# Kernel optimization log

Hardware: AMD Instinct MI355X
Metric: run time of the kernel (lower is better)

The kernel has to match this reference:

```python
import jax, jax.numpy as jnp
import numpy as np

TOP_K = 32

def setup_inputs() -> dict:
    key = jax.random.key(0)
    x = jax.random.normal(key, (4096, 32768), dtype=jnp.float32)
    return {"x": x}

def reference(x) -> jnp.ndarray:
    bsz, d_sae = x.shape
    k = min(TOP_K, d_sae)
    # top-k indices per row (unsorted order does not matter for masking)
    _, idxs = jax.lax.top_k(x, k)  # [batch, k]
    rows = jnp.arange(bsz)[:, None]  # [batch, 1]
    mask = jnp.zeros_like(x).at[rows, idxs].set(1.0)
    return mask * x
```

## Files before the change

kernel.cpp:

```cpp
#include <hip/hip_runtime.h>

#define TOPK    32
#define ROW     32768
#define THREADS 512
#define WAVES   8
#define VPT     16
#define BINS    2048
#define CAP     1024

__device__ __forceinline__ unsigned int f2key(float f) {
    unsigned int u = __float_as_uint(f);
    return u ^ (0x80000000u | (unsigned int)((int)u >> 31));
}
__device__ __forceinline__ float key2f(unsigned int k) {
    unsigned int u = (k & 0x80000000u) ? (k & 0x7fffffffu) : ~k;
    return __uint_as_float(u);
}

__device__ __forceinline__ void bar_lds() {
    asm volatile("s_waitcnt lgkmcnt(0)" ::: "memory");
    __builtin_amdgcn_s_barrier();
}

struct Shared {
    unsigned int hist[BINS];
    unsigned int wsum[WAVES];
    unsigned int sel_g, sel_gabove;
    unsigned int sel_bin, sel_above;
    unsigned int cand_cnt;
    unsigned int cnt_s;
    float        cf[CAP];
    unsigned int cidx[CAP];
};

__device__ __forceinline__ void hist_select(Shared& sh, int t, int lane,
                                            int wave, unsigned int kk) {
    const int base = wave * 256 + lane * 4;
    unsigned int h0 = sh.hist[base + 0], h1 = sh.hist[base + 1];
    unsigned int h2 = sh.hist[base + 2], h3 = sh.hist[base + 3];
    unsigned int p = h0 + h1 + h2 + h3;
    unsigned int s = p;
#pragma unroll
    for (int off = 1; off < 64; off <<= 1) {
        unsigned int vv = __shfl_down(s, off);
        if (lane + off < 64) s += vv;
    }
    if (lane == 0) sh.wsum[wave] = s;
    bar_lds();

    if (t == 0) {
        unsigned int above = 0; int g = WAVES - 1;
        for (int w = WAVES - 1; w >= 0; --w) {
            if (above + sh.wsum[w] >= kk) { g = w; break; }
            above += sh.wsum[w];
        }
        sh.sel_g = (unsigned int)g; sh.sel_gabove = above;
    }
    bar_lds();

    if (wave == (int)sh.sel_g) {
        unsigned int a = sh.sel_gabove + (s - p);
        unsigned int hh[4] = {h0, h1, h2, h3};
#pragma unroll
        for (int j = 3; j >= 0; --j) {
            unsigned int h = hh[j];
            if (a < kk && a + h >= kk) {
                sh.sel_bin = (unsigned int)(base + j);
                sh.sel_above = a;
            }
            a += h;
        }
    }
    bar_lds();
}

__global__ __launch_bounds__(THREADS, 4) void topk_eager_kernel(
    const float* __restrict__ x, float* __restrict__ out) {

    __shared__ Shared sh;
    const int row  = blockIdx.x;
    const int t    = threadIdx.x;
    const int lane = t & 63;
    const int wave = t >> 6;

    const float4* __restrict__ xin =
        reinterpret_cast<const float4*>(x + (size_t)row * ROW);
    float4* __restrict__ xout =
        reinterpret_cast<float4*>(out + (size_t)row * ROW);
    float* __restrict__ orow = out + (size_t)row * ROW;

    float4 v[VPT];
    const float4 z4 = make_float4(0.f, 0.f, 0.f, 0.f);
#pragma unroll
    for (int i = 0; i < VPT; ++i) {
        v[i] = xin[i * THREADS + t];
        xout[i * THREADS + t] = z4;
    }
    __builtin_amdgcn_sched_barrier(0);

#pragma unroll
    for (int b = 0; b < BINS / THREADS; ++b) sh.hist[t + b * THREADS] = 0;
    if (t == 0) sh.cand_cnt = 0;

    float m = -__builtin_inff();
#pragma unroll
    for (int i = 0; i < VPT; ++i)
        m = fmaxf(m, fmaxf(fmaxf(v[i].x, v[i].y), fmaxf(v[i].z, v[i].w)));

    bar_lds();
    atomicAdd(&sh.hist[f2key(m) >> 21], 1u);
    bar_lds();

    hist_select(sh, t, lane, wave, TOPK);

    const float L = key2f(sh.sel_bin << 21);

#pragma unroll
    for (int i = 0; i < VPT; ++i) {
#pragma unroll
        for (int j = 0; j < 4; ++j) {
            float f = (&v[i].x)[j];
            if (f >= L) {
                unsigned int pos = atomicAdd(&sh.cand_cnt, 1u);
                if (pos < CAP) {
                    sh.cf[pos]   = f;
                    sh.cidx[pos] = (unsigned int)((i * THREADS + t) * 4 + j);
                }
            }
        }
    }
    bar_lds();
    const unsigned int C = sh.cand_cnt;

    if (C <= CAP) {
        float        wv[2];
        unsigned int wi[2];
        int nw = 0;
        for (unsigned int i = t; i < C; i += THREADS) {
            float ki = sh.cf[i]; unsigned int ii = sh.cidx[i];
            unsigned int r = 0;
            for (unsigned int j = 0; j < C; ++j) {
                float kj = sh.cf[j];
                unsigned int ij = sh.cidx[j];
                r += (kj > ki || (kj == ki && ij < ii)) ? 1u : 0u;
            }
            if (r < TOPK) { wv[nw] = ki; wi[nw] = ii; ++nw; }
        }
        __syncthreads();
        for (int q = 0; q < nw; ++q) orow[wi[q]] = wv[q];
        return;
    }

    unsigned int prefix = 0; int pbits = 0;
    unsigned int kk = TOPK, e = 0;
    for (int r = 0; r < 3; ++r) {
        const int shift = (r == 0) ? 21 : (r == 1 ? 10 : 0);
        const int bits  = (r == 2) ? 10 : 11;
        const unsigned int msk = (1u << bits) - 1u;
        bar_lds();
#pragma unroll
        for (int b = 0; b < BINS / THREADS; ++b) sh.hist[t + b * THREADS] = 0;
        bar_lds();
#pragma unroll
        for (int i = 0; i < VPT; ++i) {
#pragma unroll
            for (int j = 0; j < 4; ++j) {
                unsigned int key = f2key((&v[i].x)[j]);
                bool match = (pbits == 0) || ((key >> (32 - pbits)) == prefix);
                if (match) atomicAdd(&sh.hist[(key >> shift) & msk], 1u);
            }
        }
        bar_lds();
        hist_select(sh, t, lane, wave, kk);
        kk = kk - sh.sel_above;
        e  = sh.hist[sh.sel_bin];
        prefix = (prefix << bits) | sh.sel_bin;
        pbits += bits;
    }
    const unsigned int T = prefix;

    unsigned int Cc = ROW;
    if (e != kk) {
        unsigned int lo = 0, hi = ROW;
        while (hi - lo > 1u) {
            unsigned int mid = (lo + hi) >> 1;
            bar_lds();
            if (t == 0) sh.cnt_s = 0;
            bar_lds();
            unsigned int c = 0;
#pragma unroll
            for (int i = 0; i < VPT; ++i) {
#pragma unroll
                for (int j = 0; j < 4; ++j) {
                    unsigned int key = f2key((&v[i].x)[j]);
                    unsigned int idx = (unsigned int)((i * THREADS + t) * 4 + j);
                    if (key == T && idx < mid) ++c;
                }
            }
            if (c) atomicAdd(&sh.cnt_s, c);
            bar_lds();
            if (sh.cnt_s >= kk) hi = mid; else lo = mid;
        }
        Cc = hi;
    }

    __syncthreads();
#pragma unroll
    for (int i = 0; i < VPT; ++i) {
        float4 o;
#pragma unroll
        for (int j = 0; j < 4; ++j) {
            float f = (&v[i].x)[j];
            unsigned int key = f2key(f);
            unsigned int idx = (unsigned int)((i * THREADS + t) * 4 + j);
            (&o.x)[j] = (key > T || (key == T && idx < Cc)) ? f : 0.0f;
        }
        xout[i * THREADS + t] = o;
    }
}

extern "C" void kernel_launch(void* const* d_in, const int* in_sizes, int n_in,
                              void* d_out, int out_size, void* d_ws, size_t ws_size,
                              hipStream_t stream) {
    const float* x = (const float*)d_in[0];
    float* out = (float*)d_out;
    const int rows = in_sizes[0] / ROW;
    topk_eager_kernel<<<rows, THREADS, 0, stream>>>(x, out);
}
```

Before: 224.9 us.

## Split each row across two blocks with a workspace merge kernel

Each row is processed by two 256-thread blocks, one per half of the row. Each block zeroes its output half, finds that half's local top-32 as (key, index) pairs and writes them to workspace, and a second small kernel merges the 64 candidates per row by rank and scatters the winners. The goal is more blocks and parallelism per row, at the cost of an extra launch, workspace traffic and ordering between the zero-fill and the scatter. A single-kernel fallback is kept for when the workspace is too small, but its over-capacity path approximates the threshold and can be wrong.

```diff
diff --git a/kernel.cpp b/kernel.cpp
--- a/kernel.cpp
+++ b/kernel.cpp
@@ -2,18 +2,21 @@
 
 #define TOPK    32
 #define ROW     32768
-#define THREADS 512
-#define WAVES   8
+#define HALF    16384
+#define THREADS 256
+#define WAVES   4
 #define VPT     16
 #define BINS    2048
 #define CAP     1024
 
-__device__ __forceinline__ unsigned int f2key(float f) {
-    unsigned int u = __float_as_uint(f);
-    return u ^ (0x80000000u | (unsigned int)((int)u >> 31));
-}
-__device__ __forceinline__ float key2f(unsigned int k) {
-    unsigned int u = (k & 0x80000000u) ? (k & 0x7fffffffu) : ~k;
+typedef unsigned int u32;
+
+__device__ __forceinline__ u32 f2key(float f) {
+    u32 u = __float_as_uint(f);
+    return u ^ (0x80000000u | (u32)((int)u >> 31));
+}
+__device__ __forceinline__ float key2f(u32 k) {
+    u32 u = (k & 0x80000000u) ? (k & 0x7fffffffu) : ~k;
     return __uint_as_float(u);
 }
 
@@ -22,200 +25,319 @@
     __builtin_amdgcn_s_barrier();
 }
 
-struct Shared {
-    unsigned int hist[BINS];
-    unsigned int wsum[WAVES];
-    unsigned int sel_g, sel_gabove;
-    unsigned int sel_bin, sel_above;
-    unsigned int cand_cnt;
-    unsigned int cnt_s;
-    float        cf[CAP];
-    unsigned int cidx[CAP];
+struct SharedH {
+    u32 hist[BINS];
+    u32 wsum[WAVES];
+    u32 sel_g, sel_gabove;
+    u32 sel_bin, sel_above;
+    u32 cand_cnt;
+    u32 win_cnt;
+    u32 cnt_s;
+    u32 ckey[CAP];
+    u32 cidx[CAP];
 };
 
-__device__ __forceinline__ void hist_select(Shared& sh, int t, int lane,
-                                            int wave, unsigned int kk) {
-    const int base = wave * 256 + lane * 4;
-    unsigned int h0 = sh.hist[base + 0], h1 = sh.hist[base + 1];
-    unsigned int h2 = sh.hist[base + 2], h3 = sh.hist[base + 3];
-    unsigned int p = h0 + h1 + h2 + h3;
-    unsigned int s = p;
+__device__ __forceinline__ void hist_select(SharedH& sh, int t, int lane,
+                                            int wave, u32 kk) {
+    const int base = wave * 512 + lane * 8;
+    u32 h[8]; u32 p = 0;
+#pragma unroll
+    for (int j = 0; j < 8; ++j) { h[j] = sh.hist[base + j]; p += h[j]; }
+    u32 s = p;
 #pragma unroll
     for (int off = 1; off < 64; off <<= 1) {
-        unsigned int vv = __shfl_down(s, off);
+        u32 vv = __shfl_down(s, off);
         if (lane + off < 64) s += vv;
     }
     if (lane == 0) sh.wsum[wave] = s;
     bar_lds();
 
     if (t == 0) {
-        unsigned int above = 0; int g = WAVES - 1;
+        u32 above = 0; int g = WAVES - 1;
         for (int w = WAVES - 1; w >= 0; --w) {
             if (above + sh.wsum[w] >= kk) { g = w; break; }
             above += sh.wsum[w];
         }
-        sh.sel_g = (unsigned int)g; sh.sel_gabove = above;
+        sh.sel_g = (u32)g; sh.sel_gabove = above;
     }
     bar_lds();
 
     if (wave == (int)sh.sel_g) {
-        unsigned int a = sh.sel_gabove + (s - p);
-        unsigned int hh[4] = {h0, h1, h2, h3};
-#pragma unroll
-        for (int j = 3; j >= 0; --j) {
-            unsigned int h = hh[j];
-            if (a < kk && a + h >= kk) {
-                sh.sel_bin = (unsigned int)(base + j);
+        u32 a = sh.sel_gabove + (s - p);
+#pragma unroll
+        for (int j = 7; j >= 0; --j) {
+            u32 hh = h[j];
+            if (a < kk && a + hh >= kk) {
+                sh.sel_bin = (u32)(base + j);
                 sh.sel_above = a;
             }
-            a += h;
-        }
-    }
-    bar_lds();
-}
-
-__global__ __launch_bounds__(THREADS, 4) void topk_eager_kernel(
+            a += hh;
+        }
+    }
+    bar_lds();
+}
+
+__global__ __launch_bounds__(THREADS, 4) void topk_half_kernel(
+    const float* __restrict__ x, float* __restrict__ out,
+    uint2* __restrict__ ws) {
+
+    __shared__ SharedH sh;
+    const int hb      = blockIdx.x;
+    const int row     = hb >> 1;
+    const int halfsel = hb & 1;
+    const int t       = threadIdx.x;
+    const int lane    = t & 63;
+    const int wave    = t >> 6;
+    const size_t base_off = (size_t)row * ROW + (size_t)halfsel * HALF;
+
+    const float4* __restrict__ xin  = (const float4*)(x + base_off);
+    float4*       __restrict__ xout = (float4*)(out + base_off);
+
+    float4 v[VPT];
+    const float4 z4 = make_float4(0.f, 0.f, 0.f, 0.f);
+#pragma unroll
+    for (int i = 0; i < VPT; ++i) {
+        v[i] = xin[i * THREADS + t];
+        xout[i * THREADS + t] = z4;
+    }
+    __builtin_amdgcn_sched_barrier(0);
+
+#pragma unroll
+    for (int b = 0; b < BINS / THREADS; ++b) sh.hist[t + b * THREADS] = 0;
+    if (t == 0) { sh.cand_cnt = 0; sh.win_cnt = 0; }
+
+    float m = -__builtin_inff();
+#pragma unroll
+    for (int i = 0; i < VPT; ++i)
+        m = fmaxf(m, fmaxf(fmaxf(v[i].x, v[i].y), fmaxf(v[i].z, v[i].w)));
+
+    bar_lds();
+    atomicAdd(&sh.hist[f2key(m) >> 21], 1u);
+    bar_lds();
+
+    hist_select(sh, t, lane, wave, TOPK);
+
+    const u32 Lk = sh.sel_bin << 21;
+
+#pragma unroll
+    for (int i = 0; i < VPT; ++i) {
+#pragma unroll
+        for (int j = 0; j < 4; ++j) {
+            u32 key = f2key((&v[i].x)[j]);
+            if (key >= Lk) {
+                u32 pos = atomicAdd(&sh.cand_cnt, 1u);
+                if (pos < CAP) {
+                    sh.ckey[pos] = key;
+                    sh.cidx[pos] = (u32)((i * THREADS + t) * 4 + j);
+                }
+            }
+        }
+    }
+    bar_lds();
+    const u32 C = sh.cand_cnt;
+    uint2* __restrict__ wrow = ws + (size_t)hb * TOPK;
+
+    if (C <= CAP) {
+        for (u32 i = t; i < C; i += THREADS) {
+            u32 ki = sh.ckey[i], ii = sh.cidx[i];
+            u32 r = 0;
+            for (u32 j = 0; j < C; ++j) {
+                u32 kj = sh.ckey[j], ij = sh.cidx[j];
+                r += (kj > ki || (kj == ki && ij < ii)) ? 1u : 0u;
+            }
+            if (r < TOPK) {
+                u32 slot = atomicAdd(&sh.win_cnt, 1u);
+                wrow[slot] = make_uint2(ki, ii + (u32)halfsel * HALF);
+            }
+        }
+        return;
+    }
+
+    u32 prefix = 0; int pbits = 0;
+    u32 kk = TOPK, e = 0;
+    for (int r = 0; r < 3; ++r) {
+        const int shift = (r == 0) ? 21 : (r == 1 ? 10 : 0);
+        const int bits  = (r == 2) ? 10 : 11;
+        const u32 msk = (1u << bits) - 1u;
+        __syncthreads();
+#pragma unroll
+        for (int b = 0; b < BINS / THREADS; ++b) sh.hist[t + b * THREADS] = 0;
+        __syncthreads();
+#pragma unroll
+        for (int i = 0; i < VPT; ++i) {
+#pragma unroll
+            for (int j = 0; j < 4; ++j) {
+                u32 key = f2key((&v[i].x)[j]);
+                bool match = (pbits == 0) || ((key >> (32 - pbits)) == prefix);
+                if (match) atomicAdd(&sh.hist[(key >> shift) & msk], 1u);
+            }
+        }
+        __syncthreads();
+        if (t == 0) {
+            u32 above = 0;
+            const int nb = 1 << bits;
+            for (int b = nb - 1; b >= 0; --b) {
+                u32 h = sh.hist[b];
+                if (above + h >= kk) { sh.sel_bin = (u32)b;
+                                       sh.sel_above = above; break; }
+                above += h;
+            }
+        }
+        __syncthreads();
+        kk -= sh.sel_above;
+        e = sh.hist[sh.sel_bin];
+        prefix = (prefix << bits) | sh.sel_bin;
+        pbits += bits;
+        __syncthreads();
+    }
+    const u32 T = prefix;
+
+    u32 Cc = HALF;
+    if (e != kk) {
+        u32 lo = 0, hi = HALF;
+        while (hi - lo > 1u) {
+            u32 mid = (lo + hi) >> 1;
+            __syncthreads();
+            if (t == 0) sh.cnt_s = 0;
+            __syncthreads();
+            u32 c = 0;
+#pragma unroll
+            for (int i = 0; i < VPT; ++i) {
+#pragma unroll
+                for (int j = 0; j < 4; ++j) {
+                    u32 key = f2key((&v[i].x)[j]);
+                    u32 idx = (u32)((i * THREADS + t) * 4 + j);
+                    if (key == T && idx < mid) ++c;
+                }
+            }
+            if (c) atomicAdd(&sh.cnt_s, c);
+            __syncthreads();
+            if (sh.cnt_s >= kk) hi = mid; else lo = mid;
+        }
+        Cc = hi;
+    }
+
+#pragma unroll
+    for (int i = 0; i < VPT; ++i) {
+#pragma unroll
+        for (int j = 0; j < 4; ++j) {
+            u32 key = f2key((&v[i].x)[j]);
+            u32 idx = (u32)((i * THREADS + t) * 4 + j);
+            if (key > T || (key == T && idx < Cc)) {
+                u32 slot = atomicAdd(&sh.win_cnt, 1u);
+                wrow[slot] = make_uint2(key, idx + (u32)halfsel * HALF);
+            }
+        }
+    }
+}
+
+__global__ __launch_bounds__(64, 8) void topk_merge_kernel(
+    const uint2* __restrict__ ws, float* __restrict__ out) {
+
+    __shared__ u32 bk[64], bi[64];
+    const int row = blockIdx.x;
+    const int l   = threadIdx.x;
+
+    uint2 e = ws[(size_t)row * 64 + l];
+    bk[l] = e.x; bi[l] = e.y;
+    __syncthreads();
+
+    u32 r = 0;
+#pragma unroll
+    for (int j = 0; j < 64; ++j) {
+        u32 kj = bk[j], ij = bi[j];
+        r += (kj > e.x || (kj == e.x && ij < e.y)) ? 1u : 0u;
+    }
+    if (r < TOPK) out[(size_t)row * ROW + e.y] = key2f(e.x);
+}
+
+__global__ __launch_bounds__(512, 4) void topk_full_kernel(
     const float* __restrict__ x, float* __restrict__ out) {
 
-    __shared__ Shared sh;
+    __shared__ SharedH sh;
     const int row  = blockIdx.x;
     const int t    = threadIdx.x;
     const int lane = t & 63;
     const int wave = t >> 6;
 
-    const float4* __restrict__ xin =
+    const float4* __restrict__ xin  =
         reinterpret_cast<const float4*>(x + (size_t)row * ROW);
     float4* __restrict__ xout =
         reinterpret_cast<float4*>(out + (size_t)row * ROW);
-    float* __restrict__ orow = out + (size_t)row * ROW;
 
     float4 v[VPT];
-    const float4 z4 = make_float4(0.f, 0.f, 0.f, 0.f);
-#pragma unroll
-    for (int i = 0; i < VPT; ++i) {
-        v[i] = xin[i * THREADS + t];
-        xout[i * THREADS + t] = z4;
-    }
-    __builtin_amdgcn_sched_barrier(0);
-
-#pragma unroll
-    for (int b = 0; b < BINS / THREADS; ++b) sh.hist[t + b * THREADS] = 0;
+#pragma unroll
+    for (int i = 0; i < VPT; ++i) v[i] = xin[i * 512 + t];
+
+    for (int b = t; b < BINS; b += 512) sh.hist[b] = 0;
     if (t == 0) sh.cand_cnt = 0;
+    __syncthreads();
 
     float m = -__builtin_inff();
 #pragma unroll
     for (int i = 0; i < VPT; ++i)
         m = fmaxf(m, fmaxf(fmaxf(v[i].x, v[i].y), fmaxf(v[i].z, v[i].w)));
-
-    bar_lds();
     atomicAdd(&sh.hist[f2key(m) >> 21], 1u);
-    bar_lds();
-
-    hist_select(sh, t, lane, wave, TOPK);
-
-    const float L = key2f(sh.sel_bin << 21);
-
-#pragma unroll
-    for (int i = 0; i < VPT; ++i) {
+    __syncthreads();
+
+    if (t == 0) {
+        u32 above = 0;
+        for (int b = BINS - 1; b >= 0; --b) {
+            u32 h = sh.hist[b];
+            if (above + h >= TOPK) { sh.sel_bin = (u32)b; break; }
+            above += h;
+        }
+    }
+    __syncthreads();
+    const u32 Lk = sh.sel_bin << 21;
+
+#pragma unroll
+    for (int i = 0; i < VPT; ++i) {
+#pragma unroll
+        for (int j = 0; j < 4; ++j) {
+            u32 key = f2key((&v[i].x)[j]);
+            if (key >= Lk) {
+                u32 pos = atomicAdd(&sh.cand_cnt, 1u);
+                if (pos < CAP) {
+                    sh.ckey[pos] = key;
+                    sh.cidx[pos] = (u32)((i * 512 + t) * 4 + j);
+                }
+            }
+        }
+    }
+    __syncthreads();
+    const u32 C = sh.cand_cnt;
+    u32 Tk = 0, ic = 0;
+    if (C <= CAP) {
+        for (u32 i = t; i < C; i += 512) {
+            u32 ki = sh.ckey[i], ii = sh.cidx[i];
+            u32 r = 0;
+            for (u32 j = 0; j < C; ++j) {
+                u32 kj = sh.ckey[j], ij = sh.cidx[j];
+                r += (kj > ki || (kj == ki && ij < ii)) ? 1u : 0u;
+            }
+            if (r == TOPK - 1) { sh.sel_g = ki; sh.sel_gabove = ii; }
+        }
+        __syncthreads();
+        Tk = sh.sel_g; ic = sh.sel_gabove;
+    } else {
+        if (t == 0) {
+            sh.sel_g = Lk; sh.sel_gabove = ROW;
+        }
+        __syncthreads();
+        Tk = sh.sel_g; ic = sh.sel_gabove;
+    }
+#pragma unroll
+    for (int i = 0; i < VPT; ++i) {
+        float4 o;
 #pragma unroll
         for (int j = 0; j < 4; ++j) {
             float f = (&v[i].x)[j];
-            if (f >= L) {
-                unsigned int pos = atomicAdd(&sh.cand_cnt, 1u);
-                if (pos < CAP) {
-                    sh.cf[pos]   = f;
-                    sh.cidx[pos] = (unsigned int)((i * THREADS + t) * 4 + j);
-                }
-            }
-        }
-    }
-    bar_lds();
-    const unsigned int C = sh.cand_cnt;
-
-    if (C <= CAP) {
-        float        wv[2];
-        unsigned int wi[2];
-        int nw = 0;
-        for (unsigned int i = t; i < C; i += THREADS) {
-            float ki = sh.cf[i]; unsigned int ii = sh.cidx[i];
-            unsigned int r = 0;
-            for (unsigned int j = 0; j < C; ++j) {
-                float kj = sh.cf[j];
-                unsigned int ij = sh.cidx[j];
-                r += (kj > ki || (kj == ki && ij < ii)) ? 1u : 0u;
-            }
-            if (r < TOPK) { wv[nw] = ki; wi[nw] = ii; ++nw; }
-        }
-        __syncthreads();
-        for (int q = 0; q < nw; ++q) orow[wi[q]] = wv[q];
-        return;
-    }
-
-    unsigned int prefix = 0; int pbits = 0;
-    unsigned int kk = TOPK, e = 0;
-    for (int r = 0; r < 3; ++r) {
-        const int shift = (r == 0) ? 21 : (r == 1 ? 10 : 0);
-        const int bits  = (r == 2) ? 10 : 11;
-        const unsigned int msk = (1u << bits) - 1u;
-        bar_lds();
-#pragma unroll
-        for (int b = 0; b < BINS / THREADS; ++b) sh.hist[t + b * THREADS] = 0;
-        bar_lds();
-#pragma unroll
-        for (int i = 0; i < VPT; ++i) {
-#pragma unroll
-            for (int j = 0; j < 4; ++j) {
-                unsigned int key = f2key((&v[i].x)[j]);
-                bool match = (pbits == 0) || ((key >> (32 - pbits)) == prefix);
-                if (match) atomicAdd(&sh.hist[(key >> shift) & msk], 1u);
-            }
-        }
-        bar_lds();
-        hist_select(sh, t, lane, wave, kk);
-        kk = kk - sh.sel_above;
-        e  = sh.hist[sh.sel_bin];
-        prefix = (prefix << bits) | sh.sel_bin;
-        pbits += bits;
-    }
-    const unsigned int T = prefix;
-
-    unsigned int Cc = ROW;
-    if (e != kk) {
-        unsigned int lo = 0, hi = ROW;
-        while (hi - lo > 1u) {
-            unsigned int mid = (lo + hi) >> 1;
-            bar_lds();
-            if (t == 0) sh.cnt_s = 0;
-            bar_lds();
-            unsigned int c = 0;
-#pragma unroll
-            for (int i = 0; i < VPT; ++i) {
-#pragma unroll
-                for (int j = 0; j < 4; ++j) {
-                    unsigned int key = f2key((&v[i].x)[j]);
-                    unsigned int idx = (unsigned int)((i * THREADS + t) * 4 + j);
-                    if (key == T && idx < mid) ++c;
-                }
-            }
-            if (c) atomicAdd(&sh.cnt_s, c);
-            bar_lds();
-            if (sh.cnt_s >= kk) hi = mid; else lo = mid;
-        }
-        Cc = hi;
-    }
-
-    __syncthreads();
-#pragma unroll
-    for (int i = 0; i < VPT; ++i) {
-        float4 o;
-#pragma unroll
-        for (int j = 0; j < 4; ++j) {
-            float f = (&v[i].x)[j];
-            unsigned int key = f2key(f);
-            unsigned int idx = (unsigned int)((i * THREADS + t) * 4 + j);
-            (&o.x)[j] = (key > T || (key == T && idx < Cc)) ? f : 0.0f;
-        }
-        xout[i * THREADS + t] = o;
+            u32 key = f2key(f);
+            u32 idx = (u32)((i * 512 + t) * 4 + j);
+            (&o.x)[j] = (key > Tk || (key == Tk && idx <= ic)) ? f : 0.0f;
+        }
+        xout[i * 512 + t] = o;
     }
 }
 
@@ -225,5 +347,12 @@
     const float* x = (const float*)d_in[0];
     float* out = (float*)d_out;
     const int rows = in_sizes[0] / ROW;
-    topk_eager_kernel<<<rows, THREADS, 0, stream>>>(x, out);
-}
+    const size_t need = (size_t)rows * 2 * TOPK * sizeof(uint2);
+    if (ws_size >= need) {
+        uint2* ws = (uint2*)d_ws;
+        topk_half_kernel<<<rows * 2, THREADS, 0, stream>>>(x, out, ws);
+        topk_merge_kernel<<<rows, 64, 0, stream>>>(ws, out);
+    } else {
+        topk_full_kernel<<<rows, 512, 0, stream>>>(x, out);
+    }
+}
```

After: 257.1 us. +14.3%, slower.

## Persistent blocks with staggered start and single-pass masked write

Applied to the files above, without the earlier changes.

Switches to 512 persistent blocks that each process several rows. On every CU, every second block, chosen through a hardware-ID ticket in workspace memory, spins in a dummy FMA loop before starting, so that load and compute phases of co-resident blocks fall out of phase. The fast path no longer zero-fills the output up front and then scatters winners; it finds the 32nd value and its index cutoff and writes the masked row in one pass, removing a full extra store of the output. This adds a memset launch and deliberate idle time, and depends on the HW_ID/XCC_ID register layout.

```diff
diff --git a/kernel.cpp b/kernel.cpp
--- a/kernel.cpp
+++ b/kernel.cpp
@@ -7,13 +7,17 @@
 #define VPT     16
 #define BINS    2048
 #define CAP     1024
-
-__device__ __forceinline__ unsigned int f2key(float f) {
-    unsigned int u = __float_as_uint(f);
-    return u ^ (0x80000000u | (unsigned int)((int)u >> 31));
-}
-__device__ __forceinline__ float key2f(unsigned int k) {
-    unsigned int u = (k & 0x80000000u) ? (k & 0x7fffffffu) : ~k;
+#define NBLK    512
+#define DELAY_ITERS 3600
+
+typedef unsigned int u32;
+
+__device__ __forceinline__ u32 f2key(float f) {
+    u32 u = __float_as_uint(f);
+    return u ^ (0x80000000u | (u32)((int)u >> 31));
+}
+__device__ __forceinline__ float key2f(u32 k) {
+    u32 u = (k & 0x80000000u) ? (k & 0x7fffffffu) : ~k;
     return __uint_as_float(u);
 }
 
@@ -23,49 +27,52 @@
 }
 
 struct Shared {
-    unsigned int hist[BINS];
-    unsigned int wsum[WAVES];
-    unsigned int sel_g, sel_gabove;
-    unsigned int sel_bin, sel_above;
-    unsigned int cand_cnt;
-    unsigned int cnt_s;
-    float        cf[CAP];
-    unsigned int cidx[CAP];
+    u32 hist[BINS];
+    u32 wsum[WAVES];
+    u32 sel_g, sel_gabove;
+    u32 sel_bin, sel_above;
+    u32 cand_cnt;
+    u32 cnt_s;
+    float Tf;
+    u32 idxcut;
+    u32 delay;
+    float ckey[CAP];
+    u32 cidx[CAP];
 };
 
 __device__ __forceinline__ void hist_select(Shared& sh, int t, int lane,
-                                            int wave, unsigned int kk) {
+                                            int wave, u32 kk) {
     const int base = wave * 256 + lane * 4;
-    unsigned int h0 = sh.hist[base + 0], h1 = sh.hist[base + 1];
-    unsigned int h2 = sh.hist[base + 2], h3 = sh.hist[base + 3];
-    unsigned int p = h0 + h1 + h2 + h3;
-    unsigned int s = p;
+    u32 h0 = sh.hist[base + 0], h1 = sh.hist[base + 1];
+    u32 h2 = sh.hist[base + 2], h3 = sh.hist[base + 3];
+    u32 p = h0 + h1 + h2 + h3;
+    u32 s = p;
 #pragma unroll
     for (int off = 1; off < 64; off <<= 1) {
-        unsigned int vv = __shfl_down(s, off);
+        u32 vv = __shfl_down(s, off);
         if (lane + off < 64) s += vv;
     }
     if (lane == 0) sh.wsum[wave] = s;
     bar_lds();
 
     if (t == 0) {
-        unsigned int above = 0; int g = WAVES - 1;
+        u32 above = 0; int g = WAVES - 1;
         for (int w = WAVES - 1; w >= 0; --w) {
             if (above + sh.wsum[w] >= kk) { g = w; break; }
             above += sh.wsum[w];
         }
-        sh.sel_g = (unsigned int)g; sh.sel_gabove = above;
+        sh.sel_g = (u32)g; sh.sel_gabove = above;
     }
     bar_lds();
 
     if (wave == (int)sh.sel_g) {
-        unsigned int a = sh.sel_gabove + (s - p);
-        unsigned int hh[4] = {h0, h1, h2, h3};
+        u32 a = sh.sel_gabove + (s - p);
+        u32 hh[4] = {h0, h1, h2, h3};
 #pragma unroll
         for (int j = 3; j >= 0; --j) {
-            unsigned int h = hh[j];
+            u32 h = hh[j];
             if (a < kk && a + h >= kk) {
-                sh.sel_bin = (unsigned int)(base + j);
+                sh.sel_bin = (u32)(base + j);
                 sh.sel_above = a;
             }
             a += h;
@@ -74,29 +81,16 @@
     bar_lds();
 }
 
-__global__ __launch_bounds__(THREADS, 4) void topk_eager_kernel(
-    const float* __restrict__ x, float* __restrict__ out) {
-
-    __shared__ Shared sh;
-    const int row  = blockIdx.x;
-    const int t    = threadIdx.x;
-    const int lane = t & 63;
-    const int wave = t >> 6;
-
-    const float4* __restrict__ xin =
-        reinterpret_cast<const float4*>(x + (size_t)row * ROW);
-    float4* __restrict__ xout =
-        reinterpret_cast<float4*>(out + (size_t)row * ROW);
-    float* __restrict__ orow = out + (size_t)row * ROW;
+__device__ __forceinline__ void process_row(Shared& sh,
+                                            const float* __restrict__ xrow,
+                                            float* __restrict__ orow,
+                                            int t, int lane, int wave) {
+    const float4* __restrict__ xin  = (const float4*)xrow;
+    float4*       __restrict__ xout = (float4*)orow;
 
     float4 v[VPT];
-    const float4 z4 = make_float4(0.f, 0.f, 0.f, 0.f);
-#pragma unroll
-    for (int i = 0; i < VPT; ++i) {
-        v[i] = xin[i * THREADS + t];
-        xout[i * THREADS + t] = z4;
-    }
-    __builtin_amdgcn_sched_barrier(0);
+#pragma unroll
+    for (int i = 0; i < VPT; ++i) v[i] = xin[i * THREADS + t];
 
 #pragma unroll
     for (int b = 0; b < BINS / THREADS; ++b) sh.hist[t + b * THREADS] = 0;
@@ -121,42 +115,51 @@
         for (int j = 0; j < 4; ++j) {
             float f = (&v[i].x)[j];
             if (f >= L) {
-                unsigned int pos = atomicAdd(&sh.cand_cnt, 1u);
+                u32 pos = atomicAdd(&sh.cand_cnt, 1u);
                 if (pos < CAP) {
-                    sh.cf[pos]   = f;
-                    sh.cidx[pos] = (unsigned int)((i * THREADS + t) * 4 + j);
+                    sh.ckey[pos] = f;
+                    sh.cidx[pos] = (u32)((i * THREADS + t) * 4 + j);
                 }
             }
         }
     }
     bar_lds();
-    const unsigned int C = sh.cand_cnt;
+    const u32 C = sh.cand_cnt;
 
     if (C <= CAP) {
-        float        wv[2];
-        unsigned int wi[2];
-        int nw = 0;
-        for (unsigned int i = t; i < C; i += THREADS) {
-            float ki = sh.cf[i]; unsigned int ii = sh.cidx[i];
-            unsigned int r = 0;
-            for (unsigned int j = 0; j < C; ++j) {
-                float kj = sh.cf[j];
-                unsigned int ij = sh.cidx[j];
+        for (u32 i = t; i < C; i += THREADS) {
+            float ki = sh.ckey[i]; u32 ii = sh.cidx[i];
+            u32 r = 0;
+            for (u32 j = 0; j < C; ++j) {
+                float kj = sh.ckey[j];
+                u32 ij = sh.cidx[j];
                 r += (kj > ki || (kj == ki && ij < ii)) ? 1u : 0u;
             }
-            if (r < TOPK) { wv[nw] = ki; wi[nw] = ii; ++nw; }
-        }
-        __syncthreads();
-        for (int q = 0; q < nw; ++q) orow[wi[q]] = wv[q];
+            if (r == TOPK - 1) { sh.Tf = ki; sh.idxcut = ii; }
+        }
+        bar_lds();
+        const float T = sh.Tf;
+        const u32 ic = sh.idxcut;
+#pragma unroll
+        for (int i = 0; i < VPT; ++i) {
+            float4 o;
+#pragma unroll
+            for (int j = 0; j < 4; ++j) {
+                float f = (&v[i].x)[j];
+                u32 idx = (u32)((i * THREADS + t) * 4 + j);
+                (&o.x)[j] = (f > T || (f == T && idx <= ic)) ? f : 0.0f;
+            }
+            xout[i * THREADS + t] = o;
+        }
         return;
     }
 
-    unsigned int prefix = 0; int pbits = 0;
-    unsigned int kk = TOPK, e = 0;
+    u32 prefix = 0; int pbits = 0;
+    u32 kk = TOPK, e = 0;
     for (int r = 0; r < 3; ++r) {
         const int shift = (r == 0) ? 21 : (r == 1 ? 10 : 0);
         const int bits  = (r == 2) ? 10 : 11;
-        const unsigned int msk = (1u << bits) - 1u;
+        const u32 msk = (1u << bits) - 1u;
         bar_lds();
 #pragma unroll
         for (int b = 0; b < BINS / THREADS; ++b) sh.hist[t + b * THREADS] = 0;
@@ -165,7 +168,7 @@
         for (int i = 0; i < VPT; ++i) {
 #pragma unroll
             for (int j = 0; j < 4; ++j) {
-                unsigned int key = f2key((&v[i].x)[j]);
+                u32 key = f2key((&v[i].x)[j]);
                 bool match = (pbits == 0) || ((key >> (32 - pbits)) == prefix);
                 if (match) atomicAdd(&sh.hist[(key >> shift) & msk], 1u);
             }
@@ -177,23 +180,23 @@
         prefix = (prefix << bits) | sh.sel_bin;
         pbits += bits;
     }
-    const unsigned int T = prefix;
-
-    unsigned int Cc = ROW;
+    const u32 T = prefix;
+
+    u32 Cc = ROW;
     if (e != kk) {
-        unsigned int lo = 0, hi = ROW;
+        u32 lo = 0, hi = ROW;
         while (hi - lo > 1u) {
-            unsigned int mid = (lo + hi) >> 1;
+            u32 mid = (lo + hi) >> 1;
             bar_lds();
             if (t == 0) sh.cnt_s = 0;
             bar_lds();
-            unsigned int c = 0;
+            u32 c = 0;
 #pragma unroll
             for (int i = 0; i < VPT; ++i) {
 #pragma unroll
                 for (int j = 0; j < 4; ++j) {
-                    unsigned int key = f2key((&v[i].x)[j]);
-                    unsigned int idx = (unsigned int)((i * THREADS + t) * 4 + j);
+                    u32 key = f2key((&v[i].x)[j]);
+                    u32 idx = (u32)((i * THREADS + t) * 4 + j);
                     if (key == T && idx < mid) ++c;
                 }
             }
@@ -204,18 +207,51 @@
         Cc = hi;
     }
 
-    __syncthreads();
 #pragma unroll
     for (int i = 0; i < VPT; ++i) {
         float4 o;
 #pragma unroll
         for (int j = 0; j < 4; ++j) {
             float f = (&v[i].x)[j];
-            unsigned int key = f2key(f);
-            unsigned int idx = (unsigned int)((i * THREADS + t) * 4 + j);
+            u32 key = f2key(f);
+            u32 idx = (u32)((i * THREADS + t) * 4 + j);
             (&o.x)[j] = (key > T || (key == T && idx < Cc)) ? f : 0.0f;
         }
         xout[i * THREADS + t] = o;
+    }
+}
+
+__global__ __launch_bounds__(THREADS, 4) void topk_stagger_kernel(
+    const float* __restrict__ x, float* __restrict__ out,
+    u32* __restrict__ tickets, int rpb, int nrows) {
+
+    __shared__ Shared sh;
+    const int t    = threadIdx.x;
+    const int lane = t & 63;
+    const int wave = t >> 6;
+
+    if (t == 0) {
+        u32 hwid = 0, xcc = 0;
+        asm volatile("s_getreg_b32 %0, hwreg(HW_REG_HW_ID)" : "=s"(hwid));
+        asm volatile("s_getreg_b32 %0, hwreg(HW_REG_XCC_ID)" : "=s"(xcc));
+        u32 slot = ((xcc & 0xFu) << 8) | ((hwid >> 8) & 0xFFu);
+        sh.delay = atomicAdd(&tickets[slot], 1u) & 1u;
+    }
+    __syncthreads();
+    if (sh.delay) {
+        float acc = 1.0f + (float)t * 1e-12f;
+        for (int i = 0; i < DELAY_ITERS; ++i)
+            acc = __builtin_fmaf(acc, 1.0000001f, 1e-9f);
+        asm volatile("" :: "v"(acc));
+    }
+
+    const int row0 = blockIdx.x * rpb;
+    for (int r = 0; r < rpb; ++r) {
+        const int row = row0 + r;
+        if (row >= nrows) break;
+        bar_lds();
+        process_row(sh, x + (size_t)row * ROW, out + (size_t)row * ROW,
+                    t, lane, wave);
     }
 }
 
@@ -225,5 +261,8 @@
     const float* x = (const float*)d_in[0];
     float* out = (float*)d_out;
     const int rows = in_sizes[0] / ROW;
-    topk_eager_kernel<<<rows, THREADS, 0, stream>>>(x, out);
-}
+    const int rpb  = (rows + NBLK - 1) / NBLK;
+    hipMemsetAsync(d_ws, 0, 4096 * sizeof(u32), stream);
+    topk_stagger_kernel<<<NBLK, THREADS, 0, stream>>>(
+        x, out, (u32*)d_ws, rpb, rows);
+}
```

After: 401.4 us. 78.5% more time.
